# Performance work log

Measured on AMD Instinct MI355X. Metric: run time of the kernel, lower is better.

## Reference

```python
import jax, jax.numpy as jnp
import numpy as np

B, Cin, H, W = 4, 64, 160, 160
Cout, K, STRIDE, PAD = 64, 3, 1, 1
KK = K * K


def setup_inputs() -> dict:
    key = jax.random.key(0)
    ks = jax.random.split(key, 4)
    x = jax.random.normal(ks[0], (B, Cin, H, W), jnp.float32)
    # offset/mask conv params (zero-init in source; small random so offsets are non-trivial)
    offset_w = jax.random.normal(ks[1], (3 * KK, Cin, K, K), jnp.float32) * 0.01
    offset_b = jax.random.normal(ks[2], (3 * KK,), jnp.float32) * 0.01
    fan_in = Cin * K * K
    weight = jax.random.normal(ks[3], (Cout, Cin, K, K), jnp.float32) / np.sqrt(fan_in)
    bias = jnp.zeros((Cout,), jnp.float32)
    return dict(x=x, offset_w=offset_w, offset_b=offset_b, weight=weight, bias=bias)


def _conv2d(x, w, b):
    y = jax.lax.conv_general_dilated(
        x, w, window_strides=(STRIDE, STRIDE),
        padding=[(PAD, PAD), (PAD, PAD)],
        dimension_numbers=('NCHW', 'OIHW', 'NCHW'))
    return y + b[None, :, None, None]


def _deform_conv2d(x, offset, mask, weight, bias):
    # x: [B,C,H,W]; offset: [B,2*KK,Ho,Wo] as (dy,dx) pairs; mask: [B,KK,Ho,Wo]
    Bs, C, Hh, Ww = x.shape
    Ho, Wo = offset.shape[2], offset.shape[3]
    off = offset.reshape(Bs, KK, 2, Ho, Wo)
    dy, dx = off[:, :, 0], off[:, :, 1]            # [B,KK,Ho,Wo]
    ki, kj = jnp.meshgrid(jnp.arange(K), jnp.arange(K), indexing='ij')
    ki = ki.reshape(KK).astype(jnp.float32)
    kj = kj.reshape(KK).astype(jnp.float32)
    hb = (jnp.arange(Ho) * STRIDE - PAD).astype(jnp.float32)
    wb = (jnp.arange(Wo) * STRIDE - PAD).astype(jnp.float32)
    py = dy + ki[None, :, None, None] + hb[None, None, :, None]  # sample y coords
    px = dx + kj[None, :, None, None] + wb[None, None, None, :]  # sample x coords
    y0 = jnp.floor(py); x0 = jnp.floor(px)
    wy1 = py - y0; wy0 = 1.0 - wy1
    wx1 = px - x0; wx0 = 1.0 - wx1
    x_hwc = jnp.transpose(x, (0, 2, 3, 1))          # [B,H,W,C]

    def corner(yc, xc):
        valid = (yc >= 0) & (yc < Hh) & (xc >= 0) & (xc < Ww)
        yi = jnp.clip(yc, 0, Hh - 1).astype(jnp.int32)
        xi = jnp.clip(xc, 0, Ww - 1).astype(jnp.int32)
        g = jax.vmap(lambda img, yy, xx: img[yy, xx])(x_hwc, yi, xi)  # [B,KK,Ho,Wo,C]
        return g * valid[..., None].astype(x.dtype)

    val = (corner(y0, x0) * (wy0 * wx0)[..., None]
           + corner(y0, x0 + 1.0) * (wy0 * wx1)[..., None]
           + corner(y0 + 1.0, x0) * (wy1 * wx0)[..., None]
           + corner(y0 + 1.0, x0 + 1.0) * (wy1 * wx1)[..., None])
    val = val * mask[..., None]                      # modulated (DCNv2)
    w2 = weight.reshape(weight.shape[0], C, KK)      # [O,C,KK]
    out = jnp.einsum('bkhwc,ock->bohw', val, w2)
    return out + bias[None, :, None, None]


def reference(x, offset_w, offset_b, weight, bias):
    out = _conv2d(x, offset_w, offset_b)             # [B,3*KK,Ho,Wo]
    o1, o2, m = jnp.split(out, 3, axis=1)
    offset = jnp.concatenate([o1, o2], axis=1)       # [B,2*KK,Ho,Wo]
    mask = jax.nn.sigmoid(m)
    return _deform_conv2d(x, offset, mask, weight, bias)
```

## Files before the change

kernel.cpp:

```cpp
#include <hip/hip_runtime.h>
#include <hip/hip_bf16.h>
#include <math.h>

#define B_ 4
#define CIN 64
#define H_ 160
#define W_ 160
#define COUT 64
#define KK_ 9
#define HW_ (H_ * W_)
#define KTOT 576
#define CPITCH 200
#define XPITCH 72
#define SLPITCH 17
#define NTILE 6400
#define TPX   800

typedef __attribute__((ext_vector_type(8))) short bf16x8;
typedef __attribute__((ext_vector_type(4))) float f32x4;

__device__ inline unsigned short f2bf(float f) {
    unsigned int u = __float_as_uint(f);
    u = (u + 0x7FFF + ((u >> 16) & 1)) >> 16;
    return (unsigned short)u;
}

__device__ inline unsigned short bfc(float f) {
    __hip_bfloat16 h = __float2bfloat16(f);
    union { __hip_bfloat16 h; unsigned short u; } cv;
    cv.h = h;
    return cv.u;
}

__global__ __launch_bounds__(256) void prep_all_k(const float* __restrict__ x,
                                                  const float* __restrict__ wgt,
                                                  const float* __restrict__ ow,
                                                  float* __restrict__ xt,
                                                  unsigned short* __restrict__ wB,
                                                  unsigned short* __restrict__ wB2) {
    __shared__ float tile[64][65];
    int bid = blockIdx.x;
    int t = threadIdx.x;

    if (bid < 1600) {
        int pbk = bid % 400, b = bid / 400;
        int p0 = pbk * 64;
        const float* xp = x + (size_t)b * CIN * HW_ + p0;

        int pg = (t & 15) * 4, cr = t >> 4;
#pragma unroll
        for (int i = 0; i < 4; i++) {
            int c = i * 16 + cr;
            float4 v = *(const float4*)(xp + (size_t)c * HW_ + pg);
            tile[c][pg]     = v.x;
            tile[c][pg + 1] = v.y;
            tile[c][pg + 2] = v.z;
            tile[c][pg + 3] = v.w;
        }
        __syncthreads();

        int c4 = (t & 15) * 4, pr = t >> 4;
        float* op = xt + ((size_t)b * HW_ + p0) * 64 + c4;
#pragma unroll
        for (int i = 0; i < 4; i++) {
            int p = i * 16 + pr;
            float4 v;
            v.x = tile[c4][p];
            v.y = tile[c4 + 1][p];
            v.z = tile[c4 + 2][p];
            v.w = tile[c4 + 3][p];
            *(float4*)(op + (size_t)p * 64) = v;
        }
    } else if (bid < 1744) {
        int i = (bid - 1600) * 256 + t;
        int o = i / KTOT, r = i % KTOT;
        int tap = r >> 6, c = r & 63;
        wB[i] = f2bf(wgt[(o * CIN + c) * KK_ + tap]);
    } else {
        int i = (bid - 1744) * 256 + t;
        int n = i / KTOT, r = i % KTOT;
        int tap = r >> 6, c = r & 63;
        wB2[i] = (n < 27) ? f2bf(ow[(n * CIN + c) * KK_ + tap]) : (unsigned short)0;
    }
}

__global__ __launch_bounds__(256, 8) void fused_dcn_k(const float* __restrict__ xt,
                                                      const unsigned short* __restrict__ wB2,
                                                      const float* __restrict__ ob,
                                                      const unsigned short* __restrict__ wB,
                                                      const float* __restrict__ bias,
                                                      float* __restrict__ out) {
    __shared__ __align__(16) char ubuf[7776];
    __shared__ __align__(16) char pbuf[144 * 32];
    __shared__ float slog[27 * SLPITCH];
    unsigned short* sX  = (unsigned short*)ubuf;
    unsigned short* sAc = (unsigned short*)ubuf;
    float4* spar_w = (float4*)pbuf;
    int4*   spar_o = (int4*)(pbuf + 144 * 16);

    int t = threadIdx.x;
    int lane = t & 63, wv = t >> 6;
    int bid = blockIdx.x;
    int tile = (bid & 7) * TPX + (bid >> 3);
    int gp0 = tile * 16;
    int wo0 = gp0 % W_;
    int tmp = gp0 / W_;
    int ho = tmp % H_;
    int b  = tmp / H_;

    const float* xb = xt + (size_t)b * HW_ * 64 + lane;

    for (int i = 0; i < 14; i++) {
        int r = i * 4 + wv;
        if (r < 54) {
            int yy = ho - 1 + r / 18;
            int xx = wo0 - 1 + r % 18;
            float v = 0.f;
            if (yy >= 0 && yy < H_ && xx >= 0 && xx < W_)
                v = xb[(size_t)(yy * W_ + xx) * 64];
            sX[r * XPITCH + lane] = bfc(v);
        }
    }
    __syncthreads();

    if (wv < 2) {
        int m = lane & 15, q = lane >> 4;
        int oc = wv * 16 + m;
        float bv = (oc < 27) ? ob[oc] : 0.f;
        f32x4 acc  = {bv, bv, bv, bv};
        f32x4 acc2 = {0.f, 0.f, 0.f, 0.f};
        const unsigned short* brow = wB2 + oc * KTOT + q * 8;
#pragma unroll
        for (int tap = 0; tap < 9; tap++) {
            int row = (tap / 3) * 18 + (tap % 3) + m;
            const unsigned short* sxr = sX + row * XPITCH + q * 8;
            bf16x8 af0 = *(const bf16x8*)(sxr);
            bf16x8 af1 = *(const bf16x8*)(sxr + 32);
            bf16x8 b0  = *(const bf16x8*)(brow + (2 * tap) * 32);
            bf16x8 b1  = *(const bf16x8*)(brow + (2 * tap + 1) * 32);
            acc  = __builtin_amdgcn_mfma_f32_16x16x32_bf16(af0, b0, acc,  0, 0, 0);
            acc2 = __builtin_amdgcn_mfma_f32_16x16x32_bf16(af1, b1, acc2, 0, 0, 0);
        }
#pragma unroll
        for (int r = 0; r < 4; r++) acc[r] += acc2[r];
        if (oc < 27) {
            float* sl = slog + oc * SLPITCH + q * 4;
            if (oc < 18) {
#pragma unroll
                for (int r = 0; r < 4; r++) sl[r] = acc[r];
            } else {
#pragma unroll
                for (int r = 0; r < 4; r++) sl[r] = 1.f / (1.f + expf(-acc[r]));
            }
        }
    }
    __syncthreads();

    if (lane < 36) {
        int task = lane * 4 + wv;
        int p = task & 15, k = task >> 4;
        float dyv = slog[(2 * k) * SLPITCH + p];
        float dxv = slog[(2 * k + 1) * SLPITCH + p];
        float mv  = slog[(18 + k) * SLPITCH + p];
        float py = dyv + (float)(k / 3) + (float)(ho - 1);
        float px = dxv + (float)(k % 3) + (float)(wo0 + p - 1);
        float y0f = floorf(py), x0f = floorf(px);
        float wy1 = py - y0f, wx1 = px - x0f;
        float wy0 = 1.f - wy1, wx0 = 1.f - wx1;
        int y0 = (int)y0f, x0 = (int)x0f;
        bool yv0 = (y0 >= 0) && (y0 < H_);
        bool yv1 = (y0 + 1 >= 0) && (y0 + 1 < H_);
        bool xv0 = (x0 >= 0) && (x0 < W_);
        bool xv1 = (x0 + 1 >= 0) && (x0 + 1 < W_);
        float4 w4;
        w4.x = (yv0 && xv0) ? wy0 * wx0 * mv : 0.f;
        w4.y = (yv0 && xv1) ? wy0 * wx1 * mv : 0.f;
        w4.z = (yv1 && xv0) ? wy1 * wx0 * mv : 0.f;
        w4.w = (yv1 && xv1) ? wy1 * wx1 * mv : 0.f;
        spar_w[task] = w4;
        int yc0 = min(max(y0, 0), H_ - 1), yc1 = min(max(y0 + 1, 0), H_ - 1);
        int xc0 = min(max(x0, 0), W_ - 1), xc1 = min(max(x0 + 1, 0), W_ - 1);
        int4 o4;
        o4.x = (yc0 * W_ + xc0) * 256;
        o4.y = (yc0 * W_ + xc1) * 256;
        o4.z = (yc1 * W_ + xc0) * 256;
        o4.w = (yc1 * W_ + xc1) * 256;
        spar_o[task] = o4;
    }
    __asm__ volatile("s_waitcnt lgkmcnt(0)" ::: "memory");

    int m = lane & 15, q = lane >> 4;
    int o0 = wv * 16 + m;
    float b0v = bias[o0];
    f32x4 acc0 = {b0v, b0v, b0v, b0v};
    f32x4 acc1 = {0.f, 0.f, 0.f, 0.f};
    const unsigned short* br0 = wB + o0 * KTOT + q * 8;
    const unsigned short* arow = sAc + m * CPITCH + q * 8;

    unsigned lane4 = (unsigned)lane << 2;
    const char* xu = (const char*)xt + (size_t)b * ((size_t)HW_ * 64 * 4);

#pragma unroll
    for (int c = 0; c < 3; c++) {
#pragma unroll
        for (int g = 0; g < 2; g++) {
            float v00[6], v01[6], v10[6], v11[6];
#pragma unroll
            for (int j = 0; j < 6; j++) {
                int task = 48 * c + (g * 6 + j) * 4 + wv;
                int4 o4 = spar_o[task];
                v00[j] = *(const float*)(xu + ((unsigned)o4.x + lane4));
                v01[j] = *(const float*)(xu + ((unsigned)o4.y + lane4));
                v10[j] = *(const float*)(xu + ((unsigned)o4.z + lane4));
                v11[j] = *(const float*)(xu + ((unsigned)o4.w + lane4));
            }
#pragma unroll
            for (int j = 0; j < 6; j++) {
                int task = 48 * c + (g * 6 + j) * 4 + wv;
                float4 w4 = spar_w[task];
                int p = task & 15, kc = (task >> 4) - 3 * c;
                float v = v00[j] * w4.x + v01[j] * w4.y
                        + v10[j] * w4.z + v11[j] * w4.w;
                sAc[p * CPITCH + kc * 64 + lane] = bfc(v);
            }
        }
        __syncthreads();

#pragma unroll
        for (int tl = 0; tl < 3; tl++) {
            bf16x8 af0 = *(const bf16x8*)(arow + (2 * tl) * 32);
            bf16x8 af1 = *(const bf16x8*)(arow + (2 * tl + 1) * 32);
            bf16x8 b0  = *(const bf16x8*)(br0 + ((c * 3 + tl) * 2) * 32);
            bf16x8 b1  = *(const bf16x8*)(br0 + ((c * 3 + tl) * 2 + 1) * 32);
            acc0 = __builtin_amdgcn_mfma_f32_16x16x32_bf16(af0, b0, acc0, 0, 0, 0);
            acc1 = __builtin_amdgcn_mfma_f32_16x16x32_bf16(af1, b1, acc1, 0, 0, 0);
        }
        if (c < 2) __syncthreads();
    }

#pragma unroll
    for (int r = 0; r < 4; r++) acc0[r] += acc1[r];

    size_t a0 = ((size_t)(b * COUT + o0)) * HW_ + (size_t)ho * W_ + wo0 + q * 4;
    float4 r0; r0.x = acc0[0]; r0.y = acc0[1]; r0.z = acc0[2]; r0.w = acc0[3];
    *(float4*)(out + a0) = r0;
}

extern "C" void kernel_launch(void* const* d_in, const int* in_sizes, int n_in,
                              void* d_out, int out_size, void* d_ws, size_t ws_size,
                              hipStream_t stream) {
    const float* x    = (const float*)d_in[0];
    const float* ow   = (const float*)d_in[1];
    const float* ob   = (const float*)d_in[2];
    const float* wgt  = (const float*)d_in[3];
    const float* bias = (const float*)d_in[4];
    float* out = (float*)d_out;

    float* ws  = (float*)d_ws;
    float* xt  = ws;
    unsigned short* wB  = (unsigned short*)(xt + (size_t)B_ * HW_ * CIN);
    unsigned short* wB2 = wB + (size_t)COUT * KTOT;

    prep_all_k<<<1816, 256, 0, stream>>>(x, wgt, ow, xt, wB, wB2);
    fused_dcn_k<<<NTILE, 256, 0, stream>>>(xt, wB2, ob, wB, bias, out);
}
```

Measured before the change: 198.3 us.

## Enlarge fused DCN tile from 16 to 32 output pixels per block

Each block now handles 32 consecutive output pixels instead of 16, with the input halo, offset-conv MFMA, sampling tasks and main MFMA doubled accordingly. All four waves now take part in the offset conv, and each wave computes two 16-pixel accumulator tiles that share the same weight fragments. This reuses weight loads and halo rows across more pixels and halves the block count and per-block overhead. In exchange it needs more LDS and registers, with launch bounds lowered from 8 to 5 blocks per CU, so occupancy drops.

After: 182.8 us. 1.08x faster.

```diff
diff --git a/kernel.cpp b/kernel.cpp
--- a/kernel.cpp
+++ b/kernel.cpp
@@ -10,11 +10,11 @@
 #define KK_ 9
 #define HW_ (H_ * W_)
 #define KTOT 576
-#define CPITCH 200
+#define CP32 200
 #define XPITCH 72
-#define SLPITCH 17
-#define NTILE 6400
-#define TPX   800
+#define SL32 33
+#define NT32 3200
+#define TPX32 400
 
 typedef __attribute__((ext_vector_type(8))) short bf16x8;
 typedef __attribute__((ext_vector_type(4))) float f32x4;
@@ -84,25 +84,25 @@
     }
 }
 
-__global__ __launch_bounds__(256, 8) void fused_dcn_k(const float* __restrict__ xt,
+__global__ __launch_bounds__(256, 5) void fused_dcn_k(const float* __restrict__ xt,
                                                       const unsigned short* __restrict__ wB2,
                                                       const float* __restrict__ ob,
                                                       const unsigned short* __restrict__ wB,
                                                       const float* __restrict__ bias,
                                                       float* __restrict__ out) {
-    __shared__ __align__(16) char ubuf[7776];
-    __shared__ __align__(16) char pbuf[144 * 32];
-    __shared__ float slog[27 * SLPITCH];
+    __shared__ __align__(16) char ubuf[14688];
+    __shared__ __align__(16) char pbuf[288 * 32];
+    __shared__ float slog[27 * SL32];
     unsigned short* sX  = (unsigned short*)ubuf;
     unsigned short* sAc = (unsigned short*)ubuf;
     float4* spar_w = (float4*)pbuf;
-    int4*   spar_o = (int4*)(pbuf + 144 * 16);
+    int4*   spar_o = (int4*)(pbuf + 288 * 16);
 
     int t = threadIdx.x;
     int lane = t & 63, wv = t >> 6;
     int bid = blockIdx.x;
-    int tile = (bid & 7) * TPX + (bid >> 3);
-    int gp0 = tile * 16;
+    int tile = (bid & 7) * TPX32 + (bid >> 3);
+    int gp0 = tile * 32;
     int wo0 = gp0 % W_;
     int tmp = gp0 / W_;
     int ho = tmp % H_;
@@ -110,11 +110,11 @@
 
     const float* xb = xt + (size_t)b * HW_ * 64 + lane;
 
-    for (int i = 0; i < 14; i++) {
+    for (int i = 0; i < 26; i++) {
         int r = i * 4 + wv;
-        if (r < 54) {
-            int yy = ho - 1 + r / 18;
-            int xx = wo0 - 1 + r % 18;
+        if (r < 102) {
+            int yy = ho - 1 + r / 34;
+            int xx = wo0 - 1 + r % 34;
             float v = 0.f;
             if (yy >= 0 && yy < H_ && xx >= 0 && xx < W_)
                 v = xb[(size_t)(yy * W_ + xx) * 64];
@@ -123,16 +123,17 @@
     }
     __syncthreads();
 
-    if (wv < 2) {
+    {
         int m = lane & 15, q = lane >> 4;
-        int oc = wv * 16 + m;
-        float bv = (oc < 27) ? ob[oc] : 0.f;
+        int h  = wv >> 1;
+        int ocl = (wv & 1) * 16 + m;
+        float bv = (ocl < 27) ? ob[ocl] : 0.f;
         f32x4 acc  = {bv, bv, bv, bv};
         f32x4 acc2 = {0.f, 0.f, 0.f, 0.f};
-        const unsigned short* brow = wB2 + oc * KTOT + q * 8;
+        const unsigned short* brow = wB2 + ocl * KTOT + q * 8;
 #pragma unroll
         for (int tap = 0; tap < 9; tap++) {
-            int row = (tap / 3) * 18 + (tap % 3) + m;
+            int row = (tap / 3) * 34 + (tap % 3) + h * 16 + m;
             const unsigned short* sxr = sX + row * XPITCH + q * 8;
             bf16x8 af0 = *(const bf16x8*)(sxr);
             bf16x8 af1 = *(const bf16x8*)(sxr + 32);
@@ -143,9 +144,9 @@
         }
 #pragma unroll
         for (int r = 0; r < 4; r++) acc[r] += acc2[r];
-        if (oc < 27) {
-            float* sl = slog + oc * SLPITCH + q * 4;
-            if (oc < 18) {
+        if (ocl < 27) {
+            float* sl = slog + ocl * SL32 + h * 16 + q * 4;
+            if (ocl < 18) {
 #pragma unroll
                 for (int r = 0; r < 4; r++) sl[r] = acc[r];
             } else {
@@ -156,12 +157,12 @@
     }
     __syncthreads();
 
-    if (lane < 36) {
-        int task = lane * 4 + wv;
-        int p = task & 15, k = task >> 4;
-        float dyv = slog[(2 * k) * SLPITCH + p];
-        float dxv = slog[(2 * k + 1) * SLPITCH + p];
-        float mv  = slog[(18 + k) * SLPITCH + p];
+    for (int l = lane; l < 72; l += 64) {
+        int task = l * 4 + wv;
+        int p = task & 31, k = task >> 5;
+        float dyv = slog[(2 * k) * SL32 + p];
+        float dxv = slog[(2 * k + 1) * SL32 + p];
+        float mv  = slog[(18 + k) * SL32 + p];
         float py = dyv + (float)(k / 3) + (float)(ho - 1);
         float px = dxv + (float)(k % 3) + (float)(wo0 + p - 1);
         float y0f = floorf(py), x0f = floorf(px);
@@ -192,10 +193,13 @@
     int m = lane & 15, q = lane >> 4;
     int o0 = wv * 16 + m;
     float b0v = bias[o0];
-    f32x4 acc0 = {b0v, b0v, b0v, b0v};
-    f32x4 acc1 = {0.f, 0.f, 0.f, 0.f};
+    f32x4 acc00 = {b0v, b0v, b0v, b0v};
+    f32x4 acc01 = {0.f, 0.f, 0.f, 0.f};
+    f32x4 acc10 = {b0v, b0v, b0v, b0v};
+    f32x4 acc11 = {0.f, 0.f, 0.f, 0.f};
     const unsigned short* br0 = wB + o0 * KTOT + q * 8;
-    const unsigned short* arow = sAc + m * CPITCH + q * 8;
+    const unsigned short* arow0 = sAc + m * CP32 + q * 8;
+    const unsigned short* arow1 = sAc + (16 + m) * CP32 + q * 8;
 
     unsigned lane4 = (unsigned)lane << 2;
     const char* xu = (const char*)xt + (size_t)b * ((size_t)HW_ * 64 * 4);
@@ -203,11 +207,11 @@
 #pragma unroll
     for (int c = 0; c < 3; c++) {
 #pragma unroll
-        for (int g = 0; g < 2; g++) {
+        for (int g = 0; g < 4; g++) {
             float v00[6], v01[6], v10[6], v11[6];
 #pragma unroll
             for (int j = 0; j < 6; j++) {
-                int task = 48 * c + (g * 6 + j) * 4 + wv;
+                int task = 96 * c + (g * 6 + j) * 4 + wv;
                 int4 o4 = spar_o[task];
                 v00[j] = *(const float*)(xu + ((unsigned)o4.x + lane4));
                 v01[j] = *(const float*)(xu + ((unsigned)o4.y + lane4));
@@ -216,34 +220,40 @@
             }
 #pragma unroll
             for (int j = 0; j < 6; j++) {
-                int task = 48 * c + (g * 6 + j) * 4 + wv;
+                int task = 96 * c + (g * 6 + j) * 4 + wv;
                 float4 w4 = spar_w[task];
-                int p = task & 15, kc = (task >> 4) - 3 * c;
+                int p = task & 31, kc = (task >> 5) - 3 * c;
                 float v = v00[j] * w4.x + v01[j] * w4.y
                         + v10[j] * w4.z + v11[j] * w4.w;
-                sAc[p * CPITCH + kc * 64 + lane] = bfc(v);
+                sAc[p * CP32 + kc * 64 + lane] = bfc(v);
             }
         }
         __syncthreads();
 
 #pragma unroll
         for (int tl = 0; tl < 3; tl++) {
-            bf16x8 af0 = *(const bf16x8*)(arow + (2 * tl) * 32);
-            bf16x8 af1 = *(const bf16x8*)(arow + (2 * tl + 1) * 32);
             bf16x8 b0  = *(const bf16x8*)(br0 + ((c * 3 + tl) * 2) * 32);
             bf16x8 b1  = *(const bf16x8*)(br0 + ((c * 3 + tl) * 2 + 1) * 32);
-            acc0 = __builtin_amdgcn_mfma_f32_16x16x32_bf16(af0, b0, acc0, 0, 0, 0);
-            acc1 = __builtin_amdgcn_mfma_f32_16x16x32_bf16(af1, b1, acc1, 0, 0, 0);
+            bf16x8 a00 = *(const bf16x8*)(arow0 + (2 * tl) * 32);
+            bf16x8 a01 = *(const bf16x8*)(arow0 + (2 * tl + 1) * 32);
+            bf16x8 a10 = *(const bf16x8*)(arow1 + (2 * tl) * 32);
+            bf16x8 a11 = *(const bf16x8*)(arow1 + (2 * tl + 1) * 32);
+            acc00 = __builtin_amdgcn_mfma_f32_16x16x32_bf16(a00, b0, acc00, 0, 0, 0);
+            acc01 = __builtin_amdgcn_mfma_f32_16x16x32_bf16(a01, b1, acc01, 0, 0, 0);
+            acc10 = __builtin_amdgcn_mfma_f32_16x16x32_bf16(a10, b0, acc10, 0, 0, 0);
+            acc11 = __builtin_amdgcn_mfma_f32_16x16x32_bf16(a11, b1, acc11, 0, 0, 0);
         }
         if (c < 2) __syncthreads();
     }
 
 #pragma unroll
-    for (int r = 0; r < 4; r++) acc0[r] += acc1[r];
+    for (int r = 0; r < 4; r++) { acc00[r] += acc01[r]; acc10[r] += acc11[r]; }
 
     size_t a0 = ((size_t)(b * COUT + o0)) * HW_ + (size_t)ho * W_ + wo0 + q * 4;
-    float4 r0; r0.x = acc0[0]; r0.y = acc0[1]; r0.z = acc0[2]; r0.w = acc0[3];
+    float4 r0; r0.x = acc00[0]; r0.y = acc00[1]; r0.z = acc00[2]; r0.w = acc00[3];
     *(float4*)(out + a0) = r0;
+    float4 r1; r1.x = acc10[0]; r1.y = acc10[1]; r1.z = acc10[2]; r1.w = acc10[3];
+    *(float4*)(out + a0 + 16) = r1;
 }
 
 extern "C" void kernel_launch(void* const* d_in, const int* in_sizes, int n_in,
@@ -262,5 +272,5 @@
     unsigned short* wB2 = wB + (size_t)COUT * KTOT;
 
     prep_all_k<<<1816, 256, 0, stream>>>(x, wgt, ow, xt, wB, wB2);
-    fused_dcn_k<<<NTILE, 256, 0, stream>>>(xt, wB2, ob, wB, bias, out);
-}
+    fused_dcn_k<<<NT32, 256, 0, stream>>>(xt, wB2, ob, wB, bias, out);
+}
```
